# Optimization experiments

Measured on AMD Instinct MI355X. Metric: run time of the kernel, lower is better.

The kernel has to match this reference:

```python
import jax, jax.numpy as jnp
import numpy as np

Nx, Ny, Nu, Np = 8, 8, 2, 4
DELTA = 0.01
P = dict(alphaA=3.5, alphaB=1.1, pho=5.0, Cp=3.0, Ar=1.0, Ab=1.0,
         kr=1.0, kb=1.0, delH1=10.0, E1byR=3000.0, k1star=2.0e4,
         Td=310.0, Qr=200.0, Qb=200.0, CAf=1.0, Tf=320.0)
YMEAN = jnp.array([0.7, 0.5, 0.5, 310.0, 0.7, 0.5, 0.5, 310.0], jnp.float32)
YSTD  = jnp.array([0.3, 0.2, 0.2, 5.0, 0.3, 0.2, 0.2, 5.0], jnp.float32)
UMEAN = jnp.array([1.0, 0.5], jnp.float32)
USTD  = jnp.array([0.1, 0.05], jnp.float32)


def _fg(x, u):
    """Grey-box CSTR+flash ODE RHS in scaled coordinates. x:(B,8), u:(B,2)."""
    x = x * YSTD + YMEAN
    u = u * USTD + UMEAN
    Hr, CAr, CBr, Tr = x[..., 0:1], x[..., 1:2], x[..., 2:3], x[..., 3:4]
    Hb, CAb, CBb, Tb = x[..., 4:5], x[..., 5:6], x[..., 6:7], x[..., 7:8]
    F, D = u[..., 0:1], u[..., 1:2]
    den = P['alphaA'] * CAb + P['alphaB'] * CBb
    CAd = P['alphaA'] * CAb / den
    CBd = P['alphaB'] * CBb / den
    Fr = P['kr'] * jnp.sqrt(Hr)
    Fb = P['kb'] * jnp.sqrt(Hb)
    k1 = P['k1star'] * jnp.exp(-P['E1byR'] / Tr)
    r1 = k1 * CAr
    dHr  = (F + D - Fr) / P['Ar']
    dCAr = (F * (P['CAf'] - CAr) + D * (CAd - CAr)) / (P['Ar'] * Hr) - r1
    dCBr = (-F * CBr + D * (CBd - CBr)) / (P['Ar'] * Hr) + r1
    dTr  = (F * (P['Tf'] - Tr) + D * (P['Td'] - Tr)) / (P['Ar'] * Hr) \
           - P['Qr'] / (P['pho'] * P['Ar'] * P['Cp'] * Hr) \
           + r1 * P['delH1'] / (P['pho'] * P['Cp'])
    dHb  = (Fr - Fb - D) / P['Ab']
    dCAb = (Fr * (CAr - CAb) + D * (CAb - CAd)) / (P['Ab'] * Hb)
    dCBb = (Fr * (CBr - CBb) + D * (CBb - CBd)) / (P['Ab'] * Hb)
    dTb  = Fr * (Tr - Tb) / (P['Ab'] * Hb) + P['Qb'] / (P['pho'] * P['Ab'] * P['Cp'] * Hb)
    xdot = jnp.concatenate([dHr, dCAr, dCBr, dTr, dHb, dCAb, dCBb, dTb], axis=-1)
    return xdot / YSTD


def _fnn(h, Ws, bs):
    for W, b in zip(Ws[:-1], bs[:-1]):
        h = jnp.tanh(h @ W + b)
    return h @ Ws[-1] + bs[-1]


def _interp(yseq):
    # (B,(Np+1)*Ny) -> midpoint interpolation -> (B, Np*Ny)
    B = yseq.shape[0]
    y = yseq.reshape(B, Np + 1, Ny)
    return (0.5 * (y[:, :-1] + y[:, 1:])).reshape(B, Np * Ny)


def _cell(Ws, bs, xGz, u):
    xG, z = xGz[:, :Nx], xGz[:, Nx:]
    ypseq, upseq = z[:, :Np * Ny], z[:, Np * Ny:]
    k1 = _fg(xG, u) + _fnn(jnp.concatenate([xG, z, u], -1), Ws, bs)
    zi = jnp.concatenate([_interp(jnp.concatenate([ypseq, xG], -1)), upseq], -1)
    x2 = xG + DELTA * (k1 / 2)
    k2 = _fg(x2, u) + _fnn(jnp.concatenate([x2, zi, u], -1), Ws, bs)
    x3 = xG + DELTA * (k2 / 2)
    k3 = _fg(x3, u) + _fnn(jnp.concatenate([x3, zi, u], -1), Ws, bs)
    ypseqShifted = jnp.concatenate([ypseq[:, Ny:], xG], -1)
    zs = jnp.concatenate([ypseqShifted, upseq], -1)
    x4 = xG + DELTA * k3
    k4 = _fg(x4, u) + _fnn(jnp.concatenate([x4, zs, u], -1), Ws, bs)
    y = xG
    xGplus = xG + (DELTA / 6.0) * (k1 + 2 * k2 + 2 * k3 + k4)
    zplus = jnp.concatenate([ypseqShifted, upseq[:, Nu:], u], -1)
    return jnp.concatenate([xGplus, zplus], -1), y


def setup_inputs() -> dict:
    key = jax.random.key(0)
    ks = jax.random.split(key, 8)
    B, T = 8192, 256
    useq = jax.random.uniform(ks[0], (B, T, Nu), dtype=jnp.float32)
    xGz0 = jax.random.uniform(ks[1], (B, Nx + Np * (Ny + Nu)), dtype=jnp.float32)
    W1 = jax.random.normal(ks[2], (50, 64), jnp.float32) * (1.0 / np.sqrt(50.0))
    b1 = jnp.zeros((64,), jnp.float32)
    W2 = jax.random.normal(ks[3], (64, 64), jnp.float32) * (1.0 / 8.0)
    b2 = jnp.zeros((64,), jnp.float32)
    W3 = jax.random.normal(ks[4], (64, 8), jnp.float32) * 1e-3  # near-zero final kernel
    b3 = jnp.zeros((8,), jnp.float32)
    return {"useq": useq, "xGz0": xGz0, "W1": W1, "b1": b1,
            "W2": W2, "b2": b2, "W3": W3, "b3": b3}


def reference(useq, xGz0, W1, b1, W2, b2, W3, b3):
    Ws, bs = (W1, W2, W3), (b1, b2, b3)
    def step(carry, u_t):
        return _cell(Ws, bs, carry, u_t)
    _, ys = jax.lax.scan(step, xGz0, jnp.swapaxes(useq, 0, 1))  # ys: (T,B,Ny)
    return jnp.swapaxes(ys, 0, 1)  # (B,T,Ny)
```

## Files before the change

kernel.cpp:

```cpp
#include <hip/hip_runtime.h>


typedef _Float16 h2_t __attribute__((ext_vector_type(2)));
typedef _Float16 h8_t __attribute__((ext_vector_type(8)));
typedef __fp16  pk2_t __attribute__((ext_vector_type(2)));
typedef float f4_t __attribute__((ext_vector_type(4)));

union H8 { h8_t v; h2_t h[4]; int i[4]; int4 i4; };
union H2I { h2_t h; pk2_t p; int i; float _f; };

#define DEVI __device__ __forceinline__

DEVI float rcp_f(float x) { return __builtin_amdgcn_rcpf(x); }
#if __has_builtin(__builtin_amdgcn_exp2f)
DEVI float exp2_f(float x) { return __builtin_amdgcn_exp2f(x); }
#else
DEVI float exp2_f(float x) { return __expf(x * 0.69314718056f); }
#endif
DEVI int pkrtz_i(float a, float b) { H2I u; u.p = __builtin_amdgcn_cvt_pkrtz(a, b); return u.i; }
DEVI h2_t pkrtz(float a, float b)  { H2I u; u.p = __builtin_amdgcn_cvt_pkrtz(a, b); return u.h; }
DEVI int bperm(int addr, int src) { return __builtin_amdgcn_ds_bpermute(addr, src); }
DEVI int h2i(h2_t h) { H2I u; u.h = h; return u.i; }

DEVI f4_t mfma16(h8_t a, h8_t b, f4_t c) {
    return __builtin_amdgcn_mfma_f32_16x16x32_f16(a, b, c, 0, 0, 0);
}

DEVI int qsel(int q, int a, int b, int c, int d) {
    int x = (q == 0) ? a : b;
    int y = (q == 2) ? c : d;
    return (q < 2) ? x : y;
}

DEVI void fg_eval(const float x[8], float F, float D, float kfg[8]) {
    float Hr  = fmaf(x[0], 0.3f, 0.7f);
    float CAr = fmaf(x[1], 0.2f, 0.5f);
    float CBr = fmaf(x[2], 0.2f, 0.5f);
    float Tr  = fmaf(x[3], 5.0f, 310.0f);
    float Hb  = fmaf(x[4], 0.3f, 0.7f);
    float CAb = fmaf(x[5], 0.2f, 0.5f);
    float CBb = fmaf(x[6], 0.2f, 0.5f);
    float Tb  = fmaf(x[7], 5.0f, 310.0f);

    float aA = 3.5f * CAb, aB = 1.1f * CBb;
    float rden = rcp_f(aA + aB);
    float CAd = aA * rden, CBd = aB * rden;
    float Fr = __builtin_amdgcn_sqrtf(Hr);
    float Fb = __builtin_amdgcn_sqrtf(Hb);
    float rTr = rcp_f(Tr);
    float k1v = 20000.0f * __expf(-3000.0f * rTr);
    float r1 = k1v * CAr;
    float rHr = rcp_f(Hr), rHb = rcp_f(Hb);

    float dHr  = F + D - Fr;
    float dCAr = (F * (1.0f - CAr) + D * (CAd - CAr)) * rHr - r1;
    float dCBr = (D * (CBd - CBr) - F * CBr) * rHr + r1;
    float dTr  = (F * (320.0f - Tr) + D * (310.0f - Tr)) * rHr
               - (40.0f / 3.0f) * rHr + (2.0f / 3.0f) * r1;
    float dHb  = Fr - Fb - D;
    float dCAb = (Fr * (CAr - CAb) + D * (CAb - CAd)) * rHb;
    float dCBb = (Fr * (CBr - CBb) + D * (CBb - CBd)) * rHb;
    float dTb  = Fr * (Tr - Tb) * rHb + (40.0f / 3.0f) * rHb;

    kfg[0] = dHr  * (10.0f / 3.0f);
    kfg[1] = dCAr * 5.0f;
    kfg[2] = dCBr * 5.0f;
    kfg[3] = dTr  * 0.2f;
    kfg[4] = dHb  * (10.0f / 3.0f);
    kfg[5] = dCAb * 5.0f;
    kfg[6] = dCBb * 5.0f;
    kfg[7] = dTb  * 0.2f;
}

struct Weights {
    h8_t a1[4][2], a2[4][2], a3[2];
    f4_t b1f[4], b2f[4], b3f;
};

DEVI void transition_lds(const f4_t acc[4], int* __restrict__ buf,
                         int wrbase, int rdbase, H8& g0, H8& g1) {
#pragma unroll
    for (int ct = 0; ct < 4; ++ct) {
        float s0 = rcp_f(1.0f + exp2_f(acc[ct][0]));
        float s1 = rcp_f(1.0f + exp2_f(acc[ct][1]));
        float s2 = rcp_f(1.0f + exp2_f(acc[ct][2]));
        float s3 = rcp_f(1.0f + exp2_f(acc[ct][3]));
        int2 pk = { pkrtz_i(s0, s1), pkrtz_i(s2, s3) };
        *(int2*)(buf + wrbase + 8 * ct) = pk;
    }
    g0.i4 = *(const int4*)(buf + rdbase);
    g1.i4 = *(const int4*)(buf + rdbase + 16);
}

DEVI void eval_stage(const float x[8], const h2_t yv[16], const h2_t up[4],
                     int upair_i, float F, float D, const Weights& W,
                     int q, int wrbase, int rdbase,
                     int* __restrict__ buf0, int* __restrict__ buf1,
                     int iN0, int iN1, float k[8]) {
    H8 f0, f1;
#pragma unroll
    for (int i = 0; i < 4; ++i) {
        int pxi = pkrtz_i(x[2 * i], x[2 * i + 1]);
        f0.i[i] = qsel(q, pxi, h2i(yv[i]), h2i(yv[4 + i]), h2i(yv[8 + i]));
        f1.i[i] = qsel(q, h2i(yv[12 + i]), h2i(up[i]),
                       (i == 0) ? upair_i : 0, 0);
    }

    f4_t a[4];
#pragma unroll
    for (int ct = 0; ct < 4; ++ct) {
        a[ct] = mfma16(W.a1[ct][0], f0.v, W.b1f[ct]);
        a[ct] = mfma16(W.a1[ct][1], f1.v, a[ct]);
    }
    H8 g0, g1;
    transition_lds(a, buf0, wrbase, rdbase, g0, g1);

#pragma unroll
    for (int ct = 0; ct < 4; ++ct) {
        a[ct] = mfma16(W.a2[ct][0], g0.v, W.b2f[ct]);
        a[ct] = mfma16(W.a2[ct][1], g1.v, a[ct]);
    }
    transition_lds(a, buf1, wrbase, rdbase, g0, g1);

    f4_t a3 = mfma16(W.a3[0], g0.v, W.b3f);
    a3 = mfma16(W.a3[1], g1.v, a3);

    float nn[8];
#pragma unroll
    for (int c = 0; c < 8; ++c) {
        int idx = (c < 4) ? iN0 : iN1;
        nn[c] = __int_as_float(bperm(idx, __float_as_int(a3[c & 3])));
    }

    float kfg[8];
    fg_eval(x, F, D, kfg);
#pragma unroll
    for (int c = 0; c < 8; ++c) k[c] = kfg[c] + nn[c];
}

__global__ __launch_bounds__(64, 1)
void cstr_mfma1_kernel(const float* __restrict__ useq, const float* __restrict__ xGz0,
                       const float* __restrict__ W1, const float* __restrict__ b1,
                       const float* __restrict__ W2, const float* __restrict__ b2,
                       const float* __restrict__ W3, const float* __restrict__ b3,
                       float* __restrict__ out)
{
    const int lane = threadIdx.x & 63;
    const int m16 = lane & 15, q = lane >> 4;
    const int b0 = blockIdx.x * 16;

    __shared__ int lds[4][16 * 36];

    const int wrbase = m16 * 36 + 2 * q;
    const int rdbase = m16 * 36 + 4 * q;
    const int iN0 = m16 << 2;
    const int iN1 = (m16 + 16) << 2;

    const float S1 = 2.0f * 1.4426950408889634f;

    Weights W;
#pragma unroll
    for (int ct = 0; ct < 4; ++ct) {
        const int mt = ct;
#pragma unroll
        for (int kh = 0; kh < 2; ++kh) {
            H8 w1f, w2f;
#pragma unroll
            for (int j = 0; j < 8; ++j) {
                int k = 32 * kh + 8 * q + j;
                int n = 16 * mt + m16;
                float v1 = (k < 50) ? S1 * W1[k * 64 + n] : 0.0f;
                float v2 = -2.0f * S1 * W2[k * 64 + n];
                ((_Float16*)&w1f)[j] = (_Float16)v1;
                ((_Float16*)&w2f)[j] = (_Float16)v2;
            }
            W.a1[ct][kh] = w1f.v;
            W.a2[ct][kh] = w2f.v;
        }
        f4_t bb1, bb2;
#pragma unroll
        for (int r = 0; r < 4; ++r) {
            int ch = 16 * mt + 4 * q + r;
            bb1[r] = S1 * b1[ch];
            float cs = 0.0f;
            for (int j = 0; j < 64; ++j) cs += W2[j * 64 + ch];
            bb2[r] = S1 * (b2[ch] + cs);
        }
        W.b1f[ct] = bb1;
        W.b2f[ct] = bb2;
    }
#pragma unroll
    for (int kh = 0; kh < 2; ++kh) {
        H8 w3f;
#pragma unroll
        for (int j = 0; j < 8; ++j) {
            int k = 32 * kh + 8 * q + j;
            ((_Float16*)&w3f)[j] = (m16 < 8) ? (_Float16)(-2.0f * W3[k * 8 + m16])
                                             : (_Float16)0.0f;
        }
        W.a3[kh] = w3f.v;
    }
    {
        f4_t bb3;
#pragma unroll
        for (int r = 0; r < 4; ++r) {
            int c = 4 * q + r;
            float v = 0.0f;
            if (c < 8) {
                float cs = 0.0f;
                for (int j = 0; j < 64; ++j) cs += W3[j * 8 + c];
                v = b3[c] + cs;
            }
            bb3[r] = v;
        }
        W.b3f = bb3;
    }

    const float* xz = xGz0 + (size_t)(b0 + m16) * 48;
    float xg[8];
#pragma unroll
    for (int c = 0; c < 8; ++c) xg[c] = xz[c];
    h2_t p[16];
#pragma unroll
    for (int i = 0; i < 16; ++i) p[i] = pkrtz(xz[8 + 2 * i], xz[9 + 2 * i]);
    h2_t up[4];
#pragma unroll
    for (int i = 0; i < 4; ++i) up[i] = pkrtz(xz[40 + 2 * i], xz[41 + 2 * i]);

    const float* ub = useq + (size_t)(b0 + m16) * 512;
    float* ob = out + (size_t)(b0 + m16) * 2048;

    float kc[8], ks[8], xv[8];

    float2 uu = *(const float2*)(ub);

#pragma unroll 1
    for (int t = 0; t < 256; ++t) {
        const float2 uun = *(const float2*)(ub + ((2 * t + 2) & 511));

        const float u0 = uu.x, u1 = uu.y;
        const float F = fmaf(u0, 0.1f, 1.0f);
        const float D = fmaf(u1, 0.05f, 0.5f);
        const int upair_i = pkrtz_i(u0, u1);

        h2_t pc[20];
#pragma unroll
        for (int i = 0; i < 16; ++i) pc[i] = p[i];
#pragma unroll
        for (int i = 0; i < 4; ++i) pc[16 + i] = pkrtz(xg[2 * i], xg[2 * i + 1]);
        h2_t pi[16], ps[16];
        const h2_t half2c = { (_Float16)0.5f, (_Float16)0.5f };
#pragma unroll
        for (int i = 0; i < 16; ++i) {
            pi[i] = (pc[i] + pc[i + 4]) * half2c;
            ps[i] = pc[i + 4];
        }

        eval_stage(xg, p,  up, upair_i, F, D, W, q, wrbase, rdbase,
                   lds[0], lds[1], iN0, iN1, kc);
#pragma unroll
        for (int c = 0; c < 8; ++c) { ks[c] = kc[c]; xv[c] = fmaf(0.005f, kc[c], xg[c]); }
        eval_stage(xv, pi, up, upair_i, F, D, W, q, wrbase, rdbase,
                   lds[2], lds[3], iN0, iN1, kc);
#pragma unroll
        for (int c = 0; c < 8; ++c) { ks[c] = fmaf(2.0f, kc[c], ks[c]); xv[c] = fmaf(0.005f, kc[c], xg[c]); }
        eval_stage(xv, pi, up, upair_i, F, D, W, q, wrbase, rdbase,
                   lds[0], lds[1], iN0, iN1, kc);
#pragma unroll
        for (int c = 0; c < 8; ++c) { ks[c] = fmaf(2.0f, kc[c], ks[c]); xv[c] = fmaf(0.01f, kc[c], xg[c]); }
        eval_stage(xv, ps, up, upair_i, F, D, W, q, wrbase, rdbase,
                   lds[2], lds[3], iN0, iN1, kc);

        {
            float s0 = (q == 0) ? xg[0] : (q == 1) ? xg[2] : (q == 2) ? xg[4] : xg[6];
            float s1 = (q == 0) ? xg[1] : (q == 1) ? xg[3] : (q == 2) ? xg[5] : xg[7];
            float2 st = { s0, s1 };
            *(float2*)(ob + t * 8 + 2 * q) = st;
        }

#pragma unroll
        for (int c = 0; c < 8; ++c) {
            ks[c] += kc[c];
            xg[c] = fmaf(0.0016666667f, ks[c], xg[c]);
        }
#pragma unroll
        for (int i = 0; i < 16; ++i) p[i] = ps[i];
        up[0] = up[1]; up[1] = up[2]; up[2] = up[3];
        { H2I u; u.i = upair_i; up[3] = u.h; }

        uu = uun;
    }
}

extern "C" void kernel_launch(void* const* d_in, const int* in_sizes, int n_in,
                              void* d_out, int out_size, void* d_ws, size_t ws_size,
                              hipStream_t stream) {
    const float* useq = (const float*)d_in[0];
    const float* xGz0 = (const float*)d_in[1];
    const float* W1   = (const float*)d_in[2];
    const float* b1   = (const float*)d_in[3];
    const float* W2   = (const float*)d_in[4];
    const float* b2   = (const float*)d_in[5];
    const float* W3   = (const float*)d_in[6];
    const float* b3   = (const float*)d_in[7];
    float* out = (float*)d_out;

    cstr_mfma1_kernel<<<dim3(512), dim3(64), 0, stream>>>(
        useq, xGz0, W1, b1, W2, b2, W3, b3, out);
}
```

Before: 978.5 us.

## Permute hidden channels so MFMA outputs feed next layer without LDS

Reorders the hidden-unit channel mapping of the W1/W2 weights and biases so that each lane's MFMA accumulator values already sit where the next MFMA's B operand needs them. The sigmoid outputs are packed straight into registers, and the LDS round-trip (writes plus reads) between layers disappears. This removes shared-memory traffic and its latency from the serial per-timestep dependency chain. Correctness relies on the permutation matching the 16x16x32 operand layout.

Result: faster. 850.8 us (-13.0%).

```diff
diff --git a/kernel.cpp b/kernel.cpp
--- a/kernel.cpp
+++ b/kernel.cpp
@@ -32,6 +32,12 @@
     return (q < 2) ? x : y;
 }
 
+DEVI int chan_of(int ct, int rho) {
+    int qr = rho >> 2, rr = rho & 3;
+    return (ct < 2) ? (8 * qr + 4 * ct + rr)
+                    : (32 + 8 * qr + 4 * (ct - 2) + rr);
+}
+
 DEVI void fg_eval(const float x[8], float F, float D, float kfg[8]) {
     float Hr  = fmaf(x[0], 0.3f, 0.7f);
     float CAr = fmaf(x[1], 0.2f, 0.5f);
@@ -77,26 +83,26 @@
     f4_t b1f[4], b2f[4], b3f;
 };
 
-DEVI void transition_lds(const f4_t acc[4], int* __restrict__ buf,
-                         int wrbase, int rdbase, H8& g0, H8& g1) {
-#pragma unroll
-    for (int ct = 0; ct < 4; ++ct) {
-        float s0 = rcp_f(1.0f + exp2_f(acc[ct][0]));
-        float s1 = rcp_f(1.0f + exp2_f(acc[ct][1]));
-        float s2 = rcp_f(1.0f + exp2_f(acc[ct][2]));
-        float s3 = rcp_f(1.0f + exp2_f(acc[ct][3]));
-        int2 pk = { pkrtz_i(s0, s1), pkrtz_i(s2, s3) };
-        *(int2*)(buf + wrbase + 8 * ct) = pk;
-    }
-    g0.i4 = *(const int4*)(buf + rdbase);
-    g1.i4 = *(const int4*)(buf + rdbase + 16);
+DEVI int sigpair(float a, float b) {
+    float s0 = rcp_f(1.0f + exp2_f(a));
+    float s1 = rcp_f(1.0f + exp2_f(b));
+    return pkrtz_i(s0, s1);
+}
+
+DEVI void transition_local(const f4_t a[4], H8& g0, H8& g1) {
+    g0.i[0] = sigpair(a[0][0], a[0][1]);
+    g0.i[1] = sigpair(a[0][2], a[0][3]);
+    g0.i[2] = sigpair(a[1][0], a[1][1]);
+    g0.i[3] = sigpair(a[1][2], a[1][3]);
+    g1.i[0] = sigpair(a[2][0], a[2][1]);
+    g1.i[1] = sigpair(a[2][2], a[2][3]);
+    g1.i[2] = sigpair(a[3][0], a[3][1]);
+    g1.i[3] = sigpair(a[3][2], a[3][3]);
 }
 
 DEVI void eval_stage(const float x[8], const h2_t yv[16], const h2_t up[4],
                      int upair_i, float F, float D, const Weights& W,
-                     int q, int wrbase, int rdbase,
-                     int* __restrict__ buf0, int* __restrict__ buf1,
-                     int iN0, int iN1, float k[8]) {
+                     int q, int iN0, int iN1, float k[8]) {
     H8 f0, f1;
 #pragma unroll
     for (int i = 0; i < 4; ++i) {
@@ -113,14 +119,14 @@
         a[ct] = mfma16(W.a1[ct][1], f1.v, a[ct]);
     }
     H8 g0, g1;
-    transition_lds(a, buf0, wrbase, rdbase, g0, g1);
+    transition_local(a, g0, g1);
 
 #pragma unroll
     for (int ct = 0; ct < 4; ++ct) {
         a[ct] = mfma16(W.a2[ct][0], g0.v, W.b2f[ct]);
         a[ct] = mfma16(W.a2[ct][1], g1.v, a[ct]);
     }
-    transition_lds(a, buf1, wrbase, rdbase, g0, g1);
+    transition_local(a, g0, g1);
 
     f4_t a3 = mfma16(W.a3[0], g0.v, W.b3f);
     a3 = mfma16(W.a3[1], g1.v, a3);
@@ -149,10 +155,6 @@
     const int m16 = lane & 15, q = lane >> 4;
     const int b0 = blockIdx.x * 16;
 
-    __shared__ int lds[4][16 * 36];
-
-    const int wrbase = m16 * 36 + 2 * q;
-    const int rdbase = m16 * 36 + 4 * q;
     const int iN0 = m16 << 2;
     const int iN1 = (m16 + 16) << 2;
 
@@ -161,14 +163,13 @@
     Weights W;
 #pragma unroll
     for (int ct = 0; ct < 4; ++ct) {
-        const int mt = ct;
+        const int n = chan_of(ct, m16);
 #pragma unroll
         for (int kh = 0; kh < 2; ++kh) {
             H8 w1f, w2f;
 #pragma unroll
             for (int j = 0; j < 8; ++j) {
                 int k = 32 * kh + 8 * q + j;
-                int n = 16 * mt + m16;
                 float v1 = (k < 50) ? S1 * W1[k * 64 + n] : 0.0f;
                 float v2 = -2.0f * S1 * W2[k * 64 + n];
                 ((_Float16*)&w1f)[j] = (_Float16)v1;
@@ -180,7 +181,7 @@
         f4_t bb1, bb2;
 #pragma unroll
         for (int r = 0; r < 4; ++r) {
-            int ch = 16 * mt + 4 * q + r;
+            int ch = chan_of(ct, 4 * q + r);
             bb1[r] = S1 * b1[ch];
             float cs = 0.0f;
             for (int j = 0; j < 64; ++j) cs += W2[j * 64 + ch];
@@ -256,20 +257,16 @@
             ps[i] = pc[i + 4];
         }
 
-        eval_stage(xg, p,  up, upair_i, F, D, W, q, wrbase, rdbase,
-                   lds[0], lds[1], iN0, iN1, kc);
+        eval_stage(xg, p,  up, upair_i, F, D, W, q, iN0, iN1, kc);
 #pragma unroll
         for (int c = 0; c < 8; ++c) { ks[c] = kc[c]; xv[c] = fmaf(0.005f, kc[c], xg[c]); }
-        eval_stage(xv, pi, up, upair_i, F, D, W, q, wrbase, rdbase,
-                   lds[2], lds[3], iN0, iN1, kc);
+        eval_stage(xv, pi, up, upair_i, F, D, W, q, iN0, iN1, kc);
 #pragma unroll
         for (int c = 0; c < 8; ++c) { ks[c] = fmaf(2.0f, kc[c], ks[c]); xv[c] = fmaf(0.005f, kc[c], xg[c]); }
-        eval_stage(xv, pi, up, upair_i, F, D, W, q, wrbase, rdbase,
-                   lds[0], lds[1], iN0, iN1, kc);
+        eval_stage(xv, pi, up, upair_i, F, D, W, q, iN0, iN1, kc);
 #pragma unroll
         for (int c = 0; c < 8; ++c) { ks[c] = fmaf(2.0f, kc[c], ks[c]); xv[c] = fmaf(0.01f, kc[c], xg[c]); }
-        eval_stage(xv, ps, up, upair_i, F, D, W, q, wrbase, rdbase,
-                   lds[2], lds[3], iN0, iN1, kc);
+        eval_stage(xv, ps, up, upair_i, F, D, W, q, iN0, iN1, kc);
 
         {
             float s0 = (q == 0) ? xg[0] : (q == 1) ? xg[2] : (q == 2) ? xg[4] : xg[6];
```
